# Optimization experiments

Hardware: AMD Instinct MI355X
Metric: run time of the kernel (lower is better)

The kernel has to match this reference:

```python
import jax, jax.numpy as jnp
import numpy as np

BN, T, D_MODEL = 128, 256, 128
D_INNER, D_STATE, D_CONV, DT_RANK = 2 * D_MODEL, 16, 4, 8  # mamba-ssm defaults


def silu(v):
    return v * jax.nn.sigmoid(v)


def setup_inputs() -> dict:
    key = jax.random.key(0)
    ks = jax.random.split(key, 8)
    s = 0.02
    A_log = jnp.log(jnp.tile(jnp.arange(1, D_STATE + 1, dtype=jnp.float32), (D_INNER, 1)))
    return {
        "x": jax.random.normal(ks[0], (BN, T, D_MODEL), jnp.float32),
        "in_proj_w": jax.random.normal(ks[1], (2 * D_INNER, D_MODEL), jnp.float32) * s,
        "conv_w": jax.random.normal(ks[2], (D_INNER, 1, D_CONV), jnp.float32) * s,
        "conv_b": jnp.zeros((D_INNER,), jnp.float32),
        "x_proj_w": jax.random.normal(ks[3], (DT_RANK + 2 * D_STATE, D_INNER), jnp.float32) * s,
        "dt_proj_w": jax.random.normal(ks[4], (D_INNER, DT_RANK), jnp.float32) * s,
        "dt_proj_b": jax.random.uniform(ks[5], (D_INNER,), jnp.float32, -4.0, -2.0),
        "A_log": A_log,
        "D": jnp.ones((D_INNER,), jnp.float32),
        "out_proj_w": jax.random.normal(ks[6], (D_MODEL, D_INNER), jnp.float32) * s,
        "down_w": jax.random.normal(ks[7], (D_MODEL, D_MODEL, 3), jnp.float32) * s,
        "down_b": jnp.zeros((D_MODEL,), jnp.float32),
        "ln_g": jnp.ones((D_MODEL,), jnp.float32),
        "ln_b": jnp.zeros((D_MODEL,), jnp.float32),
    }


def _mamba(x, in_proj_w, conv_w, conv_b, x_proj_w, dt_proj_w, dt_proj_b, A_log, D, out_proj_w):
    B = x.shape[0]
    xz = jnp.einsum('bld,ed->ble', x, in_proj_w)            # (B,L,2*di)
    xc, z = jnp.split(xz, 2, axis=-1)
    # depthwise causal conv over time
    xt = xc.transpose(0, 2, 1)                               # (B,di,L)
    xt = jax.lax.conv_general_dilated(xt, conv_w, (1,), [(D_CONV - 1, 0)],
                                      feature_group_count=D_INNER)
    xc = silu((xt + conv_b[None, :, None]).transpose(0, 2, 1))  # (B,L,di)
    x_dbl = jnp.einsum('bld,ed->ble', xc, x_proj_w)
    dt, Bm, Cm = jnp.split(x_dbl, [DT_RANK, DT_RANK + D_STATE], axis=-1)
    delta = jax.nn.softplus(jnp.einsum('blr,dr->bld', dt, dt_proj_w) + dt_proj_b)  # (B,L,di)
    A = -jnp.exp(A_log)                                       # (di,N)

    def step(h, inp):
        d_t, B_t, C_t, u_t = inp                              # (B,di),(B,N),(B,N),(B,di)
        dA = jnp.exp(d_t[..., None] * A)                      # (B,di,N)
        h = dA * h + (d_t * u_t)[..., None] * B_t[:, None, :]
        return h, jnp.einsum('bdn,bn->bd', h, C_t)

    h0 = jnp.zeros((B, D_INNER, D_STATE), x.dtype)
    _, ys = jax.lax.scan(step, h0, (delta.swapaxes(0, 1), Bm.swapaxes(0, 1),
                                    Cm.swapaxes(0, 1), xc.swapaxes(0, 1)))
    y = ys.swapaxes(0, 1) + xc * D                            # (B,L,di)
    y = y * silu(z)
    return jnp.einsum('ble,de->bld', y, out_proj_w)


def reference(x, in_proj_w, conv_w, conv_b, x_proj_w, dt_proj_w, dt_proj_b,
              A_log, D, out_proj_w, down_w, down_b, ln_g, ln_b):
    x_skip = x
    h = _mamba(x, in_proj_w, conv_w, conv_b, x_proj_w, dt_proj_w, dt_proj_b,
               A_log, D, out_proj_w)                          # dropout: eval mode = identity
    ht = h.transpose(0, 2, 1)                                 # (B,d,T)
    ht = jax.lax.conv_general_dilated(ht, down_w, (2,), [(1, 1)]) + down_b[None, :, None]
    h = ht.transpose(0, 2, 1)                                 # (B,T//2,d)
    mu = jnp.mean(h, axis=-1, keepdims=True)
    var = jnp.mean((h - mu) ** 2, axis=-1, keepdims=True)
    h = (h - mu) * jax.lax.rsqrt(var + 1e-5) * ln_g + ln_b
    return (h, x_skip)
```

## Files before the change

### kernel.cpp

```cpp
#include <hip/hip_runtime.h>
#include <hip/hip_bf16.h>


typedef __attribute__((ext_vector_type(8))) short bf16x8;
typedef __attribute__((ext_vector_type(4))) short bf16x4;
typedef __attribute__((ext_vector_type(4))) float f32x4;
using bf16 = __hip_bfloat16;

static __device__ __forceinline__ short f2s(float v) {
  union { bf16 b; short s; } u; u.b = (bf16)v; return u.s;
}
static __device__ __forceinline__ float s2f(short s) {
  union { short s; bf16 b; } u; u.s = s; return (float)u.b;
}

static __device__ __forceinline__ size_t pidx(int b, int d, int t) {
  return ((((size_t)b * 8 + (d >> 5)) * 32 + (t >> 3)) * 32 + (d & 31)) * 8 + (t & 7);
}

__global__ __launch_bounds__(256) void prep_all(const float* __restrict__ x,
                                                const float* __restrict__ ipw,
                                                const float* __restrict__ xpw,
                                                const float* __restrict__ dwn,
                                                const float* __restrict__ opw,
                                                short* __restrict__ xb,
                                                float* __restrict__ out1,
                                                short* __restrict__ ipwb,
                                                short* __restrict__ wxb,
                                                short* __restrict__ G) {
  const int bid = blockIdx.x;
  if (bid < 4096) {
    int i = (bid * 256 + threadIdx.x) * 4;
    f32x4 v = *(const f32x4*)(x + i);
    bf16x4 o;
    o[0] = f2s(v[0]); o[1] = f2s(v[1]); o[2] = f2s(v[2]); o[3] = f2s(v[3]);
    *(bf16x4*)(xb + i) = o;
    *(f32x4*)(out1 + i) = v;
  } else if (bid < 4416) {
    int idx = (bid - 4096) * 256 + threadIdx.x;
    if (idx < 65536) {
      ipwb[idx] = f2s(ipw[idx]);
    } else {
      int j = idx - 65536;
      int n = j >> 8;
      wxb[j] = (n < 40) ? f2s(xpw[j]) : (short)0;
    }
  } else {
    const int jb = bid - 4416;
    const int k  = jb >> 7;
    const int co = jb & 127;
    const int e  = threadIdx.x;
    float acc = 0.f;
    for (int dm = 0; dm < 128; ++dm) {
      acc += dwn[(co * 128 + dm) * 3 + k] * opw[dm * 256 + e];
    }
    G[(size_t)(k * 128 + co) * 256 + e] = f2s(acc);
  }
}

__global__ __launch_bounds__(256) void inproj_k(const short* __restrict__ A,
                                                const short* __restrict__ W,
                                                short* __restrict__ xcpreT,
                                                short* __restrict__ zP) {
  const int m_base = blockIdx.x * 64;
  const int n_base = blockIdx.y * 64;
  const int wave = threadIdx.x >> 6;
  const int lane = threadIdx.x & 63;
  const int r16  = lane & 15;
  const int quad = lane >> 4;
  f32x4 acc[4] = {};
  const short* Ap = A + (size_t)(m_base + wave * 16 + r16) * 128 + quad * 8;
  const short* Wp = W + (size_t)(n_base + r16) * 128 + quad * 8;
#pragma unroll
  for (int k0 = 0; k0 < 128; k0 += 32) {
    bf16x8 a = *(const bf16x8*)(Ap + k0);
#pragma unroll
    for (int j = 0; j < 4; ++j) {
      bf16x8 b = *(const bf16x8*)(Wp + (size_t)j * 16 * 128 + k0);
      acc[j] = __builtin_amdgcn_mfma_f32_16x16x32_bf16(a, b, acc[j], 0, 0, 0);
    }
  }
  __shared__ short LT[64][72];
  const bool isz = (n_base >= 256);
#pragma unroll
  for (int j = 0; j < 4; ++j) {
#pragma unroll
    for (int r = 0; r < 4; ++r) {
      float v = acc[j][r];
      short s = isz ? f2s(v / (1.f + __expf(-v))) : f2s(v);
      LT[j * 16 + r16][wave * 16 + quad * 4 + r] = s;
    }
  }
  __syncthreads();
  const int bb = m_base >> 8;
  const int tbase = m_base & 255;
  const int dbase = isz ? (n_base - 256) : n_base;
#pragma unroll
  for (int it = 0; it < 2; ++it) {
    const int dw = (threadIdx.x >> 3) + it * 32;
    const int tc = (threadIdx.x & 7) * 8;
    bf16x8 v = *(const bf16x8*)(&LT[dw][tc]);
    const int d = dbase + dw;
    const int t = tbase + tc;
    if (isz) {
      *(bf16x8*)(zP + pidx(bb, d, t)) = v;
    } else {
      *(bf16x8*)(xcpreT + ((size_t)(bb * 256 + d)) * 256 + t) = v;
    }
  }
}

__global__ __launch_bounds__(256, 4) void mid_k(const short* __restrict__ xcpreT,
                                                const float* __restrict__ cw,
                                                const float* __restrict__ cb,
                                                const short* __restrict__ wxb,
                                                const float* __restrict__ dtw,
                                                const float* __restrict__ dtb,
                                                short* __restrict__ xcP,
                                                short* __restrict__ dP,
                                                float* __restrict__ SBC) {
  const int b  = blockIdx.x >> 3;
  const int t0 = (blockIdx.x & 7) * 32;
  const int tg = threadIdx.x >> 6;
  const int dl = threadIdx.x & 63;
  const int tA = t0 + tg * 8;
  __shared__ short XC[32][264];
  __shared__ float DTL[32][8];
#pragma unroll
  for (int dtile = 0; dtile < 4; ++dtile) {
    const int d = dtile * 64 + dl;
    const float w0 = cw[d * 4], w1 = cw[d * 4 + 1];
    const float w2 = cw[d * 4 + 2], w3 = cw[d * 4 + 3];
    const float bias = cb[d];
    const size_t base = ((size_t)b * 256 + d) * 256;
    bf16x8 v = *(const bf16x8*)(xcpreT + base + tA);
    bf16x8 hp = {};
    if (tA >= 8) hp = *(const bf16x8*)(xcpreT + base + tA - 8);
    float x3 = s2f(hp[5]), x2 = s2f(hp[6]), x1 = s2f(hp[7]);
    bf16x8 outv;
#pragma unroll
    for (int i = 0; i < 8; ++i) {
      const float cur = s2f(v[i]);
      const float a = bias + x3 * w0 + x2 * w1 + x1 * w2 + cur * w3;
      const short s = f2s(a / (1.f + __expf(-a)));
      outv[i] = s;
      XC[tg * 8 + i][d] = s;
      x3 = x2; x2 = x1; x1 = cur;
    }
    *(bf16x8*)(xcP + pidx(b, d, tA)) = outv;
  }
  __syncthreads();
  if (tg < 3) {
    const int r16  = dl & 15;
    const int quad = dl >> 4;
    f32x4 acc0 = {}, acc1 = {};
    const short* Wp = wxb + (size_t)(tg * 16 + r16) * 256 + quad * 8;
#pragma unroll
    for (int k0 = 0; k0 < 256; k0 += 32) {
      bf16x8 bb = *(const bf16x8*)(Wp + k0);
      bf16x8 a0 = *(const bf16x8*)(&XC[r16][quad * 8 + k0]);
      bf16x8 a1 = *(const bf16x8*)(&XC[16 + r16][quad * 8 + k0]);
      acc0 = __builtin_amdgcn_mfma_f32_16x16x32_bf16(a0, bb, acc0, 0, 0, 0);
      acc1 = __builtin_amdgcn_mfma_f32_16x16x32_bf16(a1, bb, acc1, 0, 0, 0);
    }
    const int col = tg * 16 + r16;
#pragma unroll
    for (int r = 0; r < 4; ++r) {
      const int tl0 = quad * 4 + r;
      const int tl1 = 16 + quad * 4 + r;
      if (col < 8) {
        DTL[tl0][col] = acc0[r];
        DTL[tl1][col] = acc1[r];
      } else if (col < 40) {
        SBC[((size_t)b * 256 + t0 + tl0) * 32 + (col - 8)] = acc0[r];
        SBC[((size_t)b * 256 + t0 + tl1) * 32 + (col - 8)] = acc1[r];
      }
    }
  }
  __syncthreads();
#pragma unroll
  for (int dtile = 0; dtile < 4; ++dtile) {
    const int d = dtile * 64 + dl;
    float wd[8];
#pragma unroll
    for (int j = 0; j < 8; ++j) wd[j] = dtw[d * 8 + j];
    const float bd = dtb[d];
    bf16x8 dv;
#pragma unroll
    for (int i = 0; i < 8; ++i) {
      const int tl = tg * 8 + i;
      const f32x4 p0 = *(const f32x4*)(&DTL[tl][0]);
      const f32x4 p1 = *(const f32x4*)(&DTL[tl][4]);
      float acc = bd;
#pragma unroll
      for (int j = 0; j < 4; ++j) acc += p0[j] * wd[j] + p1[j] * wd[4 + j];
      const float delta = (acc > 20.f) ? acc : __logf(1.f + __expf(acc));
      dv[i] = f2s(delta);
    }
    *(bf16x8*)(dP + pidx(b, d, tA)) = dv;
  }
}

#define LDS_S(SB, CH) do {                                                   \
    _Pragma("unroll")                                                        \
    for (int j_ = 0; j_ < 8; ++j_) {                                         \
      SBr[SB][j_] = *(const f32x4*)(&S[(CH) * 8 + j_][q * 4]);               \
      SCr[SB][j_] = *(const f32x4*)(&S[(CH) * 8 + j_][16 + q * 4]);          \
    }                                                                        \
  } while (0)

#define LDG(GB, CH) do {                                                     \
    if ((CH) < 32) {                                                         \
      uu[GB] = *(const bf16x8*)(xcP + pb + (size_t)(CH) * 256);              \
      dd[GB] = *(const bf16x8*)(dP + pb + (size_t)(CH) * 256);               \
      if (q == 0) zz[GB] = *(const bf16x8*)(zP + pb + (size_t)(CH) * 256);   \
    }                                                                        \
  } while (0)

#define CHUNK(GB, SB, CH) do {                                               \
    _Pragma("unroll")                                                        \
    for (int tt_ = 0; tt_ < 8; ++tt_) {                                      \
      const int t_ = (CH) * 8 + tt_;                                         \
      const float delta_ = s2f(dd[GB][tt_]);                                 \
      const float u_ = s2f(uu[GB][tt_]);                                     \
      const float du_ = delta_ * u_;                                         \
      const f32x4 Bq_ = SBr[SB][tt_];                                        \
      const f32x4 Cq_ = SCr[SB][tt_];                                        \
      float yt_ = 0.f;                                                       \
      _Pragma("unroll")                                                      \
      for (int n_ = 0; n_ < 4; ++n_) {                                       \
        const float dA_ = __builtin_amdgcn_exp2f(delta_ * A2[n_]);           \
        h[n_] = dA_ * h[n_] + du_ * Bq_[n_];                                 \
        yt_ += h[n_] * Cq_[n_];                                              \
      }                                                                      \
      yt_ += __shfl_xor(yt_, 1);                                             \
      yt_ += __shfl_xor(yt_, 2);                                             \
      if (q == 0)                                                            \
        yb[(rb + t_) * 256 + d] = f2s((yt_ + u_ * Dv) * s2f(zz[GB][tt_]));   \
    }                                                                        \
  } while (0)

__global__ __launch_bounds__(128, 2) void scan12(const float* __restrict__ SBC,
                                                 const short* __restrict__ xcP,
                                                 const short* __restrict__ dP,
                                                 const short* __restrict__ zP,
                                                 const float* __restrict__ alog,
                                                 const float* __restrict__ Dp,
                                                 short* __restrict__ yb) {
  const int g = blockIdx.x & 7;
  const int b = blockIdx.x >> 3;
  const int q = threadIdx.x & 3;
  const int dl = threadIdx.x >> 2;
  const int d = g * 32 + dl;
  const size_t rb = (size_t)b * 256;
  __shared__ float S[256][32];
  for (int i = threadIdx.x; i < 2048; i += 128) {
    *(f32x4*)(&S[i >> 3][(i & 7) * 4]) =
        *(const f32x4*)(SBC + (size_t)b * 8192 + i * 4);
  }
  float A2[4];
#pragma unroll
  for (int n = 0; n < 4; ++n)
    A2[n] = -__expf(alog[d * 16 + q * 4 + n]) * 1.44269504089f;
  const float Dv = Dp[d];
  float h[4] = {0.f, 0.f, 0.f, 0.f};
  const size_t pb = (((size_t)b * 8 + g) * 32) * 256 + (size_t)dl * 8;
  f32x4 SBr[2][8], SCr[2][8];
  bf16x8 uu[4], dd[4];
  bf16x8 zz[4] = {};
  LDG(0, 0); LDG(1, 1); LDG(2, 2); LDG(3, 3);
  __syncthreads();
  LDS_S(0, 0);
  for (int c = 0; c < 32; c += 4) {
    LDS_S(1, c + 1);
    CHUNK(0, 0, c);
    LDG(0, c + 4);
    LDS_S(0, c + 2);
    CHUNK(1, 1, c + 1);
    LDG(1, c + 5);
    LDS_S(1, c + 3);
    CHUNK(2, 0, c + 2);
    LDG(2, c + 6);
    if (c + 4 < 32) LDS_S(0, c + 4);
    CHUNK(3, 1, c + 3);
    LDG(3, c + 7);
  }
}

__global__ __launch_bounds__(256) void od_k(const short* __restrict__ yb,
                                            const short* __restrict__ G,
                                            const float* __restrict__ db,
                                            const float* __restrict__ lng,
                                            const float* __restrict__ lnb,
                                            float* __restrict__ out) {
  const int wave = threadIdx.x >> 6;
  const int lane = threadIdx.x & 63;
  const int r16  = lane & 15;
  const int quad = lane >> 4;
  const int m_base = blockIdx.x * 64 + wave * 16;
  const int ma = m_base + r16;
  const int ba = ma >> 7, toa = ma & 127;
  f32x4 acc[8] = {};
  const bf16x8 az = {};
#pragma unroll
  for (int k = 0; k < 3; ++k) {
    const int tp = 2 * toa + k - 1;
    const bool valid = (tp >= 0) && (tp < 256);
    const int tpc = tp < 0 ? 0 : (tp > 255 ? 255 : tp);
    const short* Ap = yb + (size_t)(ba * 256 + tpc) * 256 + quad * 8;
    const short* Gp = G + (size_t)(k * 128 + r16) * 256 + quad * 8;
#pragma unroll
    for (int k0 = 0; k0 < 256; k0 += 32) {
      bf16x8 a = *(const bf16x8*)(Ap + k0);
      a = valid ? a : az;
#pragma unroll
      for (int j = 0; j < 8; ++j) {
        bf16x8 g = *(const bf16x8*)(Gp + (size_t)j * 16 * 256 + k0);
        acc[j] = __builtin_amdgcn_mfma_f32_16x16x32_bf16(a, g, acc[j], 0, 0, 0);
      }
    }
  }
  float dbv[8], g8[8], be8[8];
#pragma unroll
  for (int j = 0; j < 8; ++j) {
    const int col = j * 16 + r16;
    dbv[j] = db[col]; g8[j] = lng[col]; be8[j] = lnb[col];
  }
#pragma unroll
  for (int r = 0; r < 4; ++r) {
    float v[8];
    float s = 0.f;
#pragma unroll
    for (int j = 0; j < 8; ++j) { v[j] = acc[j][r] + dbv[j]; s += v[j]; }
    s += __shfl_xor(s, 1); s += __shfl_xor(s, 2);
    s += __shfl_xor(s, 4); s += __shfl_xor(s, 8);
    const float mu = s * (1.0f / 128.0f);
    float vs = 0.f;
#pragma unroll
    for (int j = 0; j < 8; ++j) { const float dd = v[j] - mu; vs += dd * dd; }
    vs += __shfl_xor(vs, 1); vs += __shfl_xor(vs, 2);
    vs += __shfl_xor(vs, 4); vs += __shfl_xor(vs, 8);
    const float rstd = rsqrtf(vs * (1.0f / 128.0f) + 1e-5f);
    const int rowm = m_base + quad * 4 + r;
#pragma unroll
    for (int j = 0; j < 8; ++j) {
      out[(size_t)rowm * 128 + j * 16 + r16] = (v[j] - mu) * rstd * g8[j] + be8[j];
    }
  }
}

static const size_t O_XCPRE = 0;
static const size_t O_XCP   = 16777216;
static const size_t O_ZP    = 33554432;
static const size_t O_DP    = 50331648;
static const size_t O_SBC   = 67108864;
static const size_t O_G     = 71303168;
static const size_t O_XB    = 75497472;
static const size_t O_IPWB  = 92274688;

extern "C" void kernel_launch(void* const* d_in, const int* in_sizes, int n_in,
                              void* d_out, int out_size, void* d_ws, size_t ws_size,
                              hipStream_t stream) {
  const float* x    = (const float*)d_in[0];
  const float* ipw  = (const float*)d_in[1];
  const float* cw   = (const float*)d_in[2];
  const float* cb   = (const float*)d_in[3];
  const float* xpw  = (const float*)d_in[4];
  const float* dtw  = (const float*)d_in[5];
  const float* dtb  = (const float*)d_in[6];
  const float* alog = (const float*)d_in[7];
  const float* Dp   = (const float*)d_in[8];
  const float* opw  = (const float*)d_in[9];
  const float* dw   = (const float*)d_in[10];
  const float* db   = (const float*)d_in[11];
  const float* lng  = (const float*)d_in[12];
  const float* lnb  = (const float*)d_in[13];

  char*  ws     = (char*)d_ws;
  short* xcpreT = (short*)(ws + O_XCPRE);
  short* yb     = (short*)(ws + O_XCPRE);
  short* xcP    = (short*)(ws + O_XCP);
  short* zP     = (short*)(ws + O_ZP);
  short* dP     = (short*)(ws + O_DP);
  float* SBC    = (float*)(ws + O_SBC);
  short* G      = (short*)(ws + O_G);
  short* xb     = (short*)(ws + O_XB);
  short* ipwb   = (short*)(ws + O_IPWB);
  float* out    = (float*)d_out;
  short* wxb    = (short*)out;
  float* out1   = out + 2097152;

  prep_all<<<4800, 256, 0, stream>>>(x, ipw, xpw, dw, opw,
                                     xb, out1, ipwb, wxb, G);
  inproj_k<<<dim3(512, 8), 256, 0, stream>>>(xb, ipwb, xcpreT, zP);
  mid_k<<<1024, 256, 0, stream>>>(xcpreT, cw, cb, wxb, dtw, dtb,
                                  xcP, dP, SBC);
  scan12<<<1024, 128, 0, stream>>>(SBC, xcP, dP, zP, alog, Dp, yb);
  od_k<<<256, 256, 0, stream>>>(yb, G, db, lng, lnb, out);
}
```

Baseline: 247.7 us.

## Fuse input projection with conv, x_proj and dt kernel into one front kernel

```diff
diff --git a/kernel.cpp b/kernel.cpp
--- a/kernel.cpp
+++ b/kernel.cpp
@@ -58,146 +58,174 @@
   }
 }
 
-__global__ __launch_bounds__(256) void inproj_k(const short* __restrict__ A,
-                                                const short* __restrict__ W,
-                                                short* __restrict__ xcpreT,
-                                                short* __restrict__ zP) {
-  const int m_base = blockIdx.x * 64;
-  const int n_base = blockIdx.y * 64;
-  const int wave = threadIdx.x >> 6;
+__global__ __launch_bounds__(256, 2) void front_k(const short* __restrict__ xb,
+                                                  const short* __restrict__ ipwb,
+                                                  const short* __restrict__ wxb,
+                                                  const float* __restrict__ cw,
+                                                  const float* __restrict__ cb,
+                                                  const float* __restrict__ dtw,
+                                                  const float* __restrict__ dtb,
+                                                  short* __restrict__ xcP,
+                                                  short* __restrict__ dP,
+                                                  short* __restrict__ zP,
+                                                  float* __restrict__ SBC) {
+  const int b  = blockIdx.x >> 2;
+  const int t0 = (blockIdx.x & 3) * 64;
+  const int w    = threadIdx.x >> 6;
   const int lane = threadIdx.x & 63;
   const int r16  = lane & 15;
   const int quad = lane >> 4;
-  f32x4 acc[4] = {};
-  const short* Ap = A + (size_t)(m_base + wave * 16 + r16) * 128 + quad * 8;
-  const short* Wp = W + (size_t)(n_base + r16) * 128 + quad * 8;
-#pragma unroll
-  for (int k0 = 0; k0 < 128; k0 += 32) {
-    bf16x8 a = *(const bf16x8*)(Ap + k0);
-#pragma unroll
-    for (int j = 0; j < 4; ++j) {
-      bf16x8 b = *(const bf16x8*)(Wp + (size_t)j * 16 * 128 + k0);
-      acc[j] = __builtin_amdgcn_mfma_f32_16x16x32_bf16(a, b, acc[j], 0, 0, 0);
-    }
-  }
+  __shared__ short AL[80][136];
+  __shared__ short XC[80][264];
   __shared__ short LT[64][72];
-  const bool isz = (n_base >= 256);
-#pragma unroll
-  for (int j = 0; j < 4; ++j) {
-#pragma unroll
-    for (int r = 0; r < 4; ++r) {
-      float v = acc[j][r];
-      short s = isz ? f2s(v / (1.f + __expf(-v))) : f2s(v);
-      LT[j * 16 + r16][wave * 16 + quad * 4 + r] = s;
-    }
-  }
-  __syncthreads();
-  const int bb = m_base >> 8;
-  const int tbase = m_base & 255;
-  const int dbase = isz ? (n_base - 256) : n_base;
-#pragma unroll
-  for (int it = 0; it < 2; ++it) {
-    const int dw = (threadIdx.x >> 3) + it * 32;
-    const int tc = (threadIdx.x & 7) * 8;
-    bf16x8 v = *(const bf16x8*)(&LT[dw][tc]);
-    const int d = dbase + dw;
-    const int t = tbase + tc;
-    if (isz) {
-      *(bf16x8*)(zP + pidx(bb, d, t)) = v;
-    } else {
-      *(bf16x8*)(xcpreT + ((size_t)(bb * 256 + d)) * 256 + t) = v;
-    }
-  }
-}
-
-__global__ __launch_bounds__(256, 4) void mid_k(const short* __restrict__ xcpreT,
-                                                const float* __restrict__ cw,
-                                                const float* __restrict__ cb,
-                                                const short* __restrict__ wxb,
-                                                const float* __restrict__ dtw,
-                                                const float* __restrict__ dtb,
-                                                short* __restrict__ xcP,
-                                                short* __restrict__ dP,
-                                                float* __restrict__ SBC) {
-  const int b  = blockIdx.x >> 3;
-  const int t0 = (blockIdx.x & 7) * 32;
-  const int tg = threadIdx.x >> 6;
-  const int dl = threadIdx.x & 63;
-  const int tA = t0 + tg * 8;
-  __shared__ short XC[32][264];
-  __shared__ float DTL[32][8];
-#pragma unroll
-  for (int dtile = 0; dtile < 4; ++dtile) {
-    const int d = dtile * 64 + dl;
+  __shared__ float DTL[64][8];
+  for (int c = threadIdx.x; c < 1280; c += 256) {
+    const int row = c >> 4;
+    const int col = (c & 15) * 8;
+    const int t = t0 - 16 + row;
+    bf16x8 v = {};
+    if (t >= 0) v = *(const bf16x8*)(xb + ((size_t)(b * 256 + t)) * 128 + col);
+    *(bf16x8*)(&AL[row][col]) = v;
+  }
+  __syncthreads();
+  {
+    f32x4 acc[5][4] = {};
+#pragma unroll
+    for (int ks = 0; ks < 4; ++ks) {
+      const int k0 = ks * 32;
+      bf16x8 wf[4];
+#pragma unroll
+      for (int j = 0; j < 4; ++j)
+        wf[j] = *(const bf16x8*)(ipwb +
+                 (size_t)(w * 64 + j * 16 + r16) * 128 + quad * 8 + k0);
+#pragma unroll
+      for (int mt = 0; mt < 5; ++mt) {
+        bf16x8 a = *(const bf16x8*)(&AL[mt * 16 + r16][quad * 8 + k0]);
+#pragma unroll
+        for (int j = 0; j < 4; ++j)
+          acc[mt][j] = __builtin_amdgcn_mfma_f32_16x16x32_bf16(a, wf[j],
+                                                               acc[mt][j], 0, 0, 0);
+      }
+    }
+#pragma unroll
+    for (int mt = 0; mt < 5; ++mt)
+#pragma unroll
+      for (int j = 0; j < 4; ++j)
+#pragma unroll
+        for (int r = 0; r < 4; ++r)
+          XC[mt * 16 + quad * 4 + r][w * 64 + j * 16 + r16] = f2s(acc[mt][j][r]);
+  }
+  for (int nt = 0; nt < 4; ++nt) {
+    f32x4 accz[4] = {};
+#pragma unroll
+    for (int ks = 0; ks < 4; ++ks) {
+      const int k0 = ks * 32;
+      bf16x8 a = *(const bf16x8*)(&AL[16 + w * 16 + r16][quad * 8 + k0]);
+#pragma unroll
+      for (int j = 0; j < 4; ++j) {
+        bf16x8 wf = *(const bf16x8*)(ipwb +
+                 (size_t)(256 + nt * 64 + j * 16 + r16) * 128 + quad * 8 + k0);
+        accz[j] = __builtin_amdgcn_mfma_f32_16x16x32_bf16(a, wf, accz[j], 0, 0, 0);
+      }
+    }
+    __syncthreads();
+#pragma unroll
+    for (int j = 0; j < 4; ++j)
+#pragma unroll
+      for (int r = 0; r < 4; ++r) {
+        float v = accz[j][r];
+        LT[j * 16 + r16][w * 16 + quad * 4 + r] = f2s(v / (1.f + __expf(-v)));
+      }
+    __syncthreads();
+#pragma unroll
+    for (int it = 0; it < 2; ++it) {
+      const int dw = (threadIdx.x >> 3) + it * 32;
+      const int tc = (threadIdx.x & 7) * 8;
+      bf16x8 v = *(const bf16x8*)(&LT[dw][tc]);
+      *(bf16x8*)(zP + pidx(b, nt * 64 + dw, t0 + tc)) = v;
+    }
+  }
+  __syncthreads();
+  bf16x8 cv[4][2];
+#pragma unroll
+  for (int dt_ = 0; dt_ < 4; ++dt_) {
+    const int d = dt_ * 64 + lane;
     const float w0 = cw[d * 4], w1 = cw[d * 4 + 1];
     const float w2 = cw[d * 4 + 2], w3 = cw[d * 4 + 3];
     const float bias = cb[d];
-    const size_t base = ((size_t)b * 256 + d) * 256;
-    bf16x8 v = *(const bf16x8*)(xcpreT + base + tA);
-    bf16x8 hp = {};
-    if (tA >= 8) hp = *(const bf16x8*)(xcpreT + base + tA - 8);
-    float x3 = s2f(hp[5]), x2 = s2f(hp[6]), x1 = s2f(hp[7]);
-    bf16x8 outv;
-#pragma unroll
-    for (int i = 0; i < 8; ++i) {
-      const float cur = s2f(v[i]);
-      const float a = bias + x3 * w0 + x2 * w1 + x1 * w2 + cur * w3;
+    const int rb_ = 16 + w * 16;
+    float p0 = s2f(XC[rb_ - 3][d]);
+    float p1 = s2f(XC[rb_ - 2][d]);
+    float p2 = s2f(XC[rb_ - 1][d]);
+#pragma unroll
+    for (int i = 0; i < 16; ++i) {
+      const float cur = s2f(XC[rb_ + i][d]);
+      const float a = bias + p0 * w0 + p1 * w1 + p2 * w2 + cur * w3;
       const short s = f2s(a / (1.f + __expf(-a)));
-      outv[i] = s;
-      XC[tg * 8 + i][d] = s;
-      x3 = x2; x2 = x1; x1 = cur;
-    }
-    *(bf16x8*)(xcP + pidx(b, d, tA)) = outv;
-  }
-  __syncthreads();
-  if (tg < 3) {
-    const int r16  = dl & 15;
-    const int quad = dl >> 4;
-    f32x4 acc0 = {}, acc1 = {};
-    const short* Wp = wxb + (size_t)(tg * 16 + r16) * 256 + quad * 8;
-#pragma unroll
-    for (int k0 = 0; k0 < 256; k0 += 32) {
-      bf16x8 bb = *(const bf16x8*)(Wp + k0);
-      bf16x8 a0 = *(const bf16x8*)(&XC[r16][quad * 8 + k0]);
-      bf16x8 a1 = *(const bf16x8*)(&XC[16 + r16][quad * 8 + k0]);
-      acc0 = __builtin_amdgcn_mfma_f32_16x16x32_bf16(a0, bb, acc0, 0, 0, 0);
-      acc1 = __builtin_amdgcn_mfma_f32_16x16x32_bf16(a1, bb, acc1, 0, 0, 0);
-    }
-    const int col = tg * 16 + r16;
-#pragma unroll
-    for (int r = 0; r < 4; ++r) {
-      const int tl0 = quad * 4 + r;
-      const int tl1 = 16 + quad * 4 + r;
-      if (col < 8) {
-        DTL[tl0][col] = acc0[r];
-        DTL[tl1][col] = acc1[r];
-      } else if (col < 40) {
-        SBC[((size_t)b * 256 + t0 + tl0) * 32 + (col - 8)] = acc0[r];
-        SBC[((size_t)b * 256 + t0 + tl1) * 32 + (col - 8)] = acc1[r];
-      }
-    }
-  }
-  __syncthreads();
-#pragma unroll
-  for (int dtile = 0; dtile < 4; ++dtile) {
-    const int d = dtile * 64 + dl;
+      cv[dt_][i >> 3][i & 7] = s;
+      p0 = p1; p1 = p2; p2 = cur;
+    }
+    *(bf16x8*)(xcP + pidx(b, d, t0 + w * 16))     = cv[dt_][0];
+    *(bf16x8*)(xcP + pidx(b, d, t0 + w * 16 + 8)) = cv[dt_][1];
+  }
+  __syncthreads();
+#pragma unroll
+  for (int dt_ = 0; dt_ < 4; ++dt_) {
+    const int d = dt_ * 64 + lane;
+#pragma unroll
+    for (int i = 0; i < 16; ++i)
+      XC[16 + w * 16 + i][d] = cv[dt_][i >> 3][i & 7];
+  }
+  __syncthreads();
+  {
+    f32x4 ax[4] = {};
+#pragma unroll
+    for (int ks = 0; ks < 8; ++ks) {
+      const int k0 = ks * 32;
+      bf16x8 a = *(const bf16x8*)(&XC[16 + w * 16 + r16][quad * 8 + k0]);
+#pragma unroll
+      for (int j = 0; j < 4; ++j) {
+        bf16x8 wf = *(const bf16x8*)(wxb + (size_t)(j * 16 + r16) * 256 + quad * 8 + k0);
+        ax[j] = __builtin_amdgcn_mfma_f32_16x16x32_bf16(a, wf, ax[j], 0, 0, 0);
+      }
+    }
+#pragma unroll
+    for (int j = 0; j < 4; ++j) {
+      const int col = j * 16 + r16;
+#pragma unroll
+      for (int r = 0; r < 4; ++r) {
+        const int tl = w * 16 + quad * 4 + r;
+        if (col < 8) {
+          DTL[tl][col] = ax[j][r];
+        } else if (col < 40) {
+          SBC[((size_t)b * 256 + t0 + tl) * 32 + (col - 8)] = ax[j][r];
+        }
+      }
+    }
+  }
+  __syncthreads();
+#pragma unroll
+  for (int dt_ = 0; dt_ < 4; ++dt_) {
+    const int d = dt_ * 64 + lane;
     float wd[8];
 #pragma unroll
     for (int j = 0; j < 8; ++j) wd[j] = dtw[d * 8 + j];
     const float bd = dtb[d];
-    bf16x8 dv;
-#pragma unroll
-    for (int i = 0; i < 8; ++i) {
-      const int tl = tg * 8 + i;
+    bf16x8 dv0, dv1;
+#pragma unroll
+    for (int i = 0; i < 16; ++i) {
+      const int tl = w * 16 + i;
       const f32x4 p0 = *(const f32x4*)(&DTL[tl][0]);
       const f32x4 p1 = *(const f32x4*)(&DTL[tl][4]);
       float acc = bd;
 #pragma unroll
       for (int j = 0; j < 4; ++j) acc += p0[j] * wd[j] + p1[j] * wd[4 + j];
       const float delta = (acc > 20.f) ? acc : __logf(1.f + __expf(acc));
-      dv[i] = f2s(delta);
-    }
-    *(bf16x8*)(dP + pidx(b, d, tA)) = dv;
+      const short s = f2s(delta);
+      if (i < 8) dv0[i] = s; else dv1[i - 8] = s;
+    }
+    *(bf16x8*)(dP + pidx(b, d, t0 + w * 16))     = dv0;
+    *(bf16x8*)(dP + pidx(b, d, t0 + w * 16 + 8)) = dv1;
   }
 }
 
@@ -349,7 +377,7 @@
   }
 }
 
-static const size_t O_XCPRE = 0;
+static const size_t O_YB    = 0;
 static const size_t O_XCP   = 16777216;
 static const size_t O_ZP    = 33554432;
 static const size_t O_DP    = 50331648;
@@ -377,8 +405,7 @@
   const float* lnb  = (const float*)d_in[13];
 
   char*  ws     = (char*)d_ws;
-  short* xcpreT = (short*)(ws + O_XCPRE);
-  short* yb     = (short*)(ws + O_XCPRE);
+  short* yb     = (short*)(ws + O_YB);
   short* xcP    = (short*)(ws + O_XCP);
   short* zP     = (short*)(ws + O_ZP);
   short* dP     = (short*)(ws + O_DP);
@@ -392,9 +419,8 @@
 
   prep_all<<<4800, 256, 0, stream>>>(x, ipw, xpw, dw, opw,
                                      xb, out1, ipwb, wxb, G);
-  inproj_k<<<dim3(512, 8), 256, 0, stream>>>(xb, ipwb, xcpreT, zP);
-  mid_k<<<1024, 256, 0, stream>>>(xcpreT, cw, cb, wxb, dtw, dtb,
-                                  xcP, dP, SBC);
+  front_k<<<512, 256, 0, stream>>>(xb, ipwb, wxb, cw, cb, dtw, dtb,
+                                   xcP, dP, zP, SBC);
   scan12<<<1024, 128, 0, stream>>>(SBC, xcP, dP, zP, alog, Dp, yb);
   od_k<<<256, 256, 0, stream>>>(yb, G, db, lng, lnb, out);
 }
```

New measurement: 225.0 us. 9.2% less time.
